# Optimization experiments

Measured on AMD Instinct MI355X. Metric: run time of the kernel, lower is better.

## Reference

```python
import jax, jax.numpy as jnp
import numpy as np

G = 8192          # graphs per hand side (PyG batch)
J_SRC = 17        # source-hand joints (transform: Linear(17*64, 13*64))
J_TGT = 13        # target-hand joints
NEG_SLOPE = 0.01  # F.leaky_relu default


def _chain_edge_index(J, num_graphs):
    # bidirectional chain tree per graph, block-diagonal batched like PyG
    p = np.arange(J - 1); c = np.arange(1, J)
    src = np.concatenate([p, c]); dst = np.concatenate([c, p])
    base = np.arange(num_graphs)[:, None] * J
    return jnp.asarray(np.stack([(src[None] + base).ravel(), (dst[None] + base).ravel()]), jnp.int32)


def _lin_init(key, o, i):
    k1, k2 = jax.random.split(key)
    s = 1.0 / np.sqrt(i)
    return (jax.random.uniform(k1, (o, i), jnp.float32, -s, s),
            jax.random.uniform(k2, (o,), jnp.float32, -s, s))


def setup_inputs() -> dict:
    key = jax.random.key(0)
    ks = iter(jax.random.split(key, 64))
    inp = {}
    Nl = G * J_SRC
    inp["l_hand_x"] = jax.random.normal(next(ks), (Nl, 3), jnp.float32)
    inp["r_hand_x"] = jax.random.normal(next(ks), (Nl, 3), jnp.float32)
    ei_src = _chain_edge_index(J_SRC, G)
    inp["l_hand_edge_index"] = ei_src
    inp["r_hand_edge_index"] = ei_src
    E_src = ei_src.shape[1]
    inp["l_hand_edge_attr"] = jax.random.normal(next(ks), (E_src, 3), jnp.float32)
    inp["r_hand_edge_attr"] = jax.random.normal(next(ks), (E_src, 3), jnp.float32)
    ei_t = _chain_edge_index(J_TGT, G)
    inp["hand_edge_index"] = ei_t
    inp["hand_edge_attr"] = jax.random.normal(next(ks), (ei_t.shape[1], 6), jnp.float32)
    Nt = G * J_TGT
    inp["hand_lower"] = -(jax.random.uniform(next(ks), (Nt, 1), jnp.float32) + 0.5)
    inp["hand_upper"] = jax.random.uniform(next(ks), (Nt, 1), jnp.float32) + 0.5
    inp["hand_offset"] = jax.random.normal(next(ks), (Nt, 3), jnp.float32) * 0.05
    ax = jax.random.normal(next(ks), (Nt, 3), jnp.float32)
    inp["hand_axis"] = ax / jnp.linalg.norm(ax, axis=-1, keepdims=True)
    par = np.concatenate([[-1], np.arange(J_TGT - 1)])  # chain: root then parents
    inp["hand_parent"] = jnp.asarray(np.tile(par, G), jnp.int32)
    inp["num_graphs"] = G
    dims = {"enc1_lin": (16, 9),  "enc1_up": (16, 3),
            "enc2_lin": (32, 35), "enc2_up": (32, 16),
            "enc3_lin": (64, 67), "enc3_up": (64, 32),
            "trans":    (13 * 64, 17 * 64),
            "dec1_lin": (32, 138), "dec1_up": (32, 66),
            "dec2_lin": (16, 70),  "dec2_up": (16, 32),
            "dec3_lin": (1, 38),   "dec3_up": (1, 16)}
    for n, (o, i) in dims.items():
        W, b = _lin_init(next(ks), o, i)
        inp[n + "_W"] = W; inp[n + "_b"] = b
    return inp


def _block(x, ei, ea, Wl, bl, Wu, bu):
    # SpatialBasicBlock: gather x_i/x_j, concat edge_attr, linear+leaky_relu,
    # scatter-add at target nodes, residual upsample of x.
    src, dst = ei[0], ei[1]
    z = jnp.concatenate([x[dst], x[src], ea], axis=-1)  # [E, 2*in+edge]
    m = jax.nn.leaky_relu(z @ Wl.T + bl, NEG_SLOPE)
    agg = jax.ops.segment_sum(m, dst, num_segments=x.shape[0])
    return agg + x @ Wu.T + bu


def _rodrigues(ax, ang):
    # rotation matrices about unit axis ax [...,3] by angle ang [...]
    c = jnp.cos(ang)[..., None, None]; s = jnp.sin(ang)[..., None, None]
    I = jnp.eye(3, dtype=ax.dtype)
    aa = ax[..., :, None] * ax[..., None, :]
    x, y, z = ax[..., 0], ax[..., 1], ax[..., 2]
    zero = jnp.zeros_like(x)
    K = jnp.stack([jnp.stack([zero, -z, y], -1),
                   jnp.stack([z, zero, -x], -1),
                   jnp.stack([-y, x, zero], -1)], -2)
    return c * I + (1 - c) * aa + s * K


def _fk(ang, parent, offset, axis, num_graphs, J):
    # forward kinematics along parent chain (parent[j] < j, root = -1)
    a = ang.reshape(num_graphs, J)
    off = offset.reshape(num_graphs, J, 3)
    ax = axis.reshape(num_graphs, J, 3)
    par = parent.reshape(num_graphs, J)[0]  # same topology in every graph
    Rl = _rodrigues(ax, a)                  # [G, J, 3, 3] local rotations
    I = jnp.eye(3, dtype=ang.dtype)
    pos = jnp.zeros((num_graphs, J, 3), ang.dtype)
    rot = jnp.zeros((num_graphs, J, 3, 3), ang.dtype)
    for j in range(J):  # J=13 fixed structural loop
        p = par[j]
        root = p < 0
        Rp = jnp.where(root, I, jnp.take(rot, p, axis=1))
        Pp = jnp.where(root, 0.0, jnp.take(pos, p, axis=1))
        pos = pos.at[:, j].set(Pp + jnp.einsum('gab,gb->ga', Rp, off[:, j]))
        rot = rot.at[:, j].set(jnp.einsum('gab,gbc->gac', Rp, Rl[:, j]))
    return pos.reshape(-1, 3)


def reference(l_hand_x, r_hand_x, l_hand_edge_index, r_hand_edge_index,
              l_hand_edge_attr, r_hand_edge_attr, hand_edge_index, hand_edge_attr,
              hand_lower, hand_upper, hand_offset, hand_axis, hand_parent, num_graphs,
              enc1_lin_W, enc1_lin_b, enc1_up_W, enc1_up_b,
              enc2_lin_W, enc2_lin_b, enc2_up_W, enc2_up_b,
              enc3_lin_W, enc3_lin_b, enc3_up_W, enc3_up_b,
              trans_W, trans_b,
              dec1_lin_W, dec1_lin_b, dec1_up_W, dec1_up_b,
              dec2_lin_W, dec2_lin_b, dec2_up_W, dec2_up_b,
              dec3_lin_W, dec3_lin_b, dec3_up_W, dec3_up_b):
    # ---- encode ----
    Nl = l_hand_x.shape[0]
    x = jnp.concatenate([l_hand_x, r_hand_x], axis=0)
    ei = jnp.concatenate([l_hand_edge_index, r_hand_edge_index + Nl], axis=1)
    ea = jnp.concatenate([l_hand_edge_attr, r_hand_edge_attr], axis=0)
    h = _block(x, ei, ea, enc1_lin_W, enc1_lin_b, enc1_up_W, enc1_up_b)
    h = _block(h, ei, ea, enc2_lin_W, enc2_lin_b, enc2_up_W, enc2_up_b)
    h = _block(h, ei, ea, enc3_lin_W, enc3_lin_b, enc3_up_W, enc3_up_b)
    G2 = 2 * num_graphs
    z = jnp.tanh(h.reshape(G2, -1) @ trans_W.T + trans_b).reshape(-1, 64)
    # ---- decode ----
    half = z.shape[0] // 2
    ei_t = jnp.concatenate([hand_edge_index, hand_edge_index + half], axis=1)
    ea_t = jnp.concatenate([hand_edge_attr, hand_edge_attr], axis=0)
    lower = jnp.concatenate([hand_lower, hand_lower], axis=0)
    upper = jnp.concatenate([hand_upper, hand_upper], axis=0)
    offset = jnp.concatenate([hand_offset, hand_offset], axis=0)
    axis = jnp.concatenate([hand_axis, hand_axis], axis=0)
    parent = jnp.concatenate([hand_parent, hand_parent], axis=0)
    xd = jnp.concatenate([z, lower, upper], axis=1)  # [2*G*13, 66]
    h = _block(xd, ei_t, ea_t, dec1_lin_W, dec1_lin_b, dec1_up_W, dec1_up_b)
    h = _block(h, ei_t, ea_t, dec2_lin_W, dec2_lin_b, dec2_up_W, dec2_up_b)
    ang = jnp.tanh(_block(h, ei_t, ea_t, dec3_lin_W, dec3_lin_b, dec3_up_W, dec3_up_b))
    ang = lower + (upper - lower) * (ang + 1) / 2
    pos = _fk(ang, parent, offset, axis, G2, J_TGT)
    hn = ang.shape[0] // 2
    return ang[:hn], pos[:hn], ang[hn:], pos[hn:]
```

## Files before the change

### kernel.cpp

```cpp
#include <hip/hip_runtime.h>
#include <math.h>


constexpr int G_NUM = 8192;
constexpr int JS = 17;
constexpr int JT = 13;
constexpr int N_ENC = 2 * G_NUM * JS;
constexpr int N_DEC = 2 * G_NUM * JT;
constexpr int G2 = 2 * G_NUM;
constexpr int HN = G_NUM * JT;
constexpr int K_TR = JS * 64;
constexpr int N_TR = JT * 64;

typedef unsigned short u16;
typedef u16   u16x8 __attribute__((ext_vector_type(8)));
typedef u16   u16x4 __attribute__((ext_vector_type(4)));
typedef float f32x4 __attribute__((ext_vector_type(4)));
typedef __bf16 bf16x8 __attribute__((ext_vector_type(8)));

__device__ __forceinline__ float lrelu(float v) { return v > 0.f ? v : 0.01f * v; }
__device__ __forceinline__ u16 f2bf(float f) {
    unsigned u = __float_as_uint(f);
    u += 0x7fff + ((u >> 16) & 1);
    return (u16)(u >> 16);
}
__device__ __forceinline__ float bf2f(u16 h) { return __uint_as_float((unsigned)h << 16); }

template<int K_MM, int C_IN_W, int C_OUT, int C_E, int J, int G, bool TAIL>
__global__ __launch_bounds__(256)
void block_mfma(const u16* __restrict__ xHi, const u16* __restrict__ xLo,
                const float* __restrict__ eaA, const float* __restrict__ eaB, int g_half,
                const float* __restrict__ lowv, const float* __restrict__ upv,
                const float* __restrict__ Wl, const float* __restrict__ bl,
                const float* __restrict__ Wu, const float* __restrict__ bu,
                u16* __restrict__ outHi, u16* __restrict__ outLo)
{
    constexpr int ROWS = G * J;
    constexpr int F = (ROWS + 15) / 16;
    constexpr int NCH = C_OUT / 16;
    constexpr int KF = K_MM / 32;
    constexpr int KPAD = K_MM + 8;
    constexpr int EAS = 2 * (J - 1) * C_E;
    constexpr int CTOT = 2 * C_IN_W + C_E;
    constexpr int CW = (C_IN_W < K_MM) ? C_IN_W : K_MM;
    constexpr int WGG = 4 * G;

    __shared__ __align__(16) u16 sWH[3 * C_OUT * KPAD], sWL[3 * C_OUT * KPAD];
    __shared__ float sEA[WGG * EAS];
    __shared__ float sWe[C_OUT * C_E];
    __shared__ float sBl[C_OUT], sBu[C_OUT];
    __shared__ float sTl[TAIL ? 6 * C_OUT : 1];
    __shared__ float sLow[TAIL ? WGG * J : 1], sUpp[TAIL ? WGG * J : 1];

    const int t = threadIdx.x;
    const int g0 = blockIdx.x * WGG;

    for (int i = t; i < 3 * C_OUT * K_MM; i += 256) {
        const int ch = i / K_MM, k = i % K_MM;
        const int p = ch / C_OUT, o = ch % C_OUT;
        float v = 0.f;
        if (k < CW) {
            if (p == 0)      v = Wl[o * CTOT + k];
            else if (p == 1) v = Wl[o * CTOT + C_IN_W + k];
            else             v = Wu[o * C_IN_W + k];
        }
        const u16 h = f2bf(v);
        sWH[ch * KPAD + k] = h;
        sWL[ch * KPAD + k] = f2bf(v - bf2f(h));
    }
    for (int i = t; i < WGG * EAS; i += 256) {
        const int lg = i / EAS, r = i % EAS;
        const int g = g0 + lg;
        sEA[i] = (g < g_half) ? eaA[(size_t)g * EAS + r]
                              : eaB[(size_t)(g - g_half) * EAS + r];
    }
    for (int i = t; i < C_OUT * C_E; i += 256)
        sWe[i] = Wl[(i / C_E) * CTOT + 2 * C_IN_W + (i % C_E)];
    if (t < C_OUT) { sBl[t] = bl[t]; sBu[t] = bu[t]; }
    if constexpr (TAIL) {
        if (t < C_OUT) {
            sTl[t * 6 + 0] = Wl[t * CTOT + K_MM];
            sTl[t * 6 + 1] = Wl[t * CTOT + K_MM + 1];
            sTl[t * 6 + 2] = Wl[t * CTOT + C_IN_W + K_MM];
            sTl[t * 6 + 3] = Wl[t * CTOT + C_IN_W + K_MM + 1];
            sTl[t * 6 + 4] = Wu[t * C_IN_W + K_MM];
            sTl[t * 6 + 5] = Wu[t * C_IN_W + K_MM + 1];
        }
        for (int i = t; i < WGG * J; i += 256) {
            const int lg = i / J, j = i % J;
            const int g = g0 + lg;
            const int ge = (g < g_half) ? g : g - g_half;
            sLow[i] = lowv[ge * J + j];
            sUpp[i] = upv[ge * J + j];
        }
    }
    __syncthreads();

    const int wv = t >> 6, lane = t & 63;
    const int col = lane & 15, kg = lane >> 4;
    const size_t baseNode = (size_t)(blockIdx.x * 4 + wv) * ROWS;
    const int lgB = wv * G;

    for (int ch = 0; ch < NCH; ++ch) {
        const int o = ch * 16 + col;
        bf16x8 wUh[KF], wUl[KF], wVh[KF], wVl[KF], wPh[KF], wPl[KF];
        #pragma unroll
        for (int kf = 0; kf < KF; ++kf) {
            wUh[kf] = *(const bf16x8*)&sWH[(0 * C_OUT + o) * KPAD + kf * 32 + kg * 8];
            wUl[kf] = *(const bf16x8*)&sWL[(0 * C_OUT + o) * KPAD + kf * 32 + kg * 8];
            wVh[kf] = *(const bf16x8*)&sWH[(1 * C_OUT + o) * KPAD + kf * 32 + kg * 8];
            wVl[kf] = *(const bf16x8*)&sWL[(1 * C_OUT + o) * KPAD + kf * 32 + kg * 8];
            wPh[kf] = *(const bf16x8*)&sWH[(2 * C_OUT + o) * KPAD + kf * 32 + kg * 8];
            wPl[kf] = *(const bf16x8*)&sWL[(2 * C_OUT + o) * KPAD + kf * 32 + kg * 8];
        }
        float we[C_E];
        #pragma unroll
        for (int k = 0; k < C_E; ++k) we[k] = sWe[o * C_E + k];
        const float blo = sBl[o], buo = sBu[o];
        float tl0 = 0, tl1 = 0, tl2 = 0, tl3 = 0, tl4 = 0, tl5 = 0;
        if constexpr (TAIL) {
            tl0 = sTl[o * 6 + 0]; tl1 = sTl[o * 6 + 1]; tl2 = sTl[o * 6 + 2];
            tl3 = sTl[o * 6 + 3]; tl4 = sTl[o * 6 + 4]; tl5 = sTl[o * 6 + 5];
        }

        f32x4 Vpp = {0,0,0,0}, Vp = {0,0,0,0};
        f32x4 Up = {0,0,0,0}, Pp = {0,0,0,0};
        #pragma unroll
        for (int f = 0; f <= F; ++f) {
            f32x4 Vc = {0,0,0,0}, Uc = {0,0,0,0}, Pc = {0,0,0,0};
            if (f < F) {
                const int nrow = f * 16 + col;
                const size_t nd = baseNode + (nrow < ROWS ? nrow : ROWS - 1);
                #pragma unroll
                for (int kf = 0; kf < KF; ++kf) {
                    const bf16x8 aH = *(const bf16x8*)&xHi[nd * K_MM + kf * 32 + kg * 8];
                    const bf16x8 aL = *(const bf16x8*)&xLo[nd * K_MM + kf * 32 + kg * 8];
                    Vc = __builtin_amdgcn_mfma_f32_16x16x32_bf16(aH, wVh[kf], Vc, 0, 0, 0);
                    Vc = __builtin_amdgcn_mfma_f32_16x16x32_bf16(aH, wVl[kf], Vc, 0, 0, 0);
                    Vc = __builtin_amdgcn_mfma_f32_16x16x32_bf16(aL, wVh[kf], Vc, 0, 0, 0);
                    Uc = __builtin_amdgcn_mfma_f32_16x16x32_bf16(aH, wUh[kf], Uc, 0, 0, 0);
                    Uc = __builtin_amdgcn_mfma_f32_16x16x32_bf16(aH, wUl[kf], Uc, 0, 0, 0);
                    Uc = __builtin_amdgcn_mfma_f32_16x16x32_bf16(aL, wUh[kf], Uc, 0, 0, 0);
                    Pc = __builtin_amdgcn_mfma_f32_16x16x32_bf16(aH, wPh[kf], Pc, 0, 0, 0);
                    Pc = __builtin_amdgcn_mfma_f32_16x16x32_bf16(aH, wPl[kf], Pc, 0, 0, 0);
                    Pc = __builtin_amdgcn_mfma_f32_16x16x32_bf16(aL, wPh[kf], Pc, 0, 0, 0);
                }
            }
            if (f >= 1) {
                const int fm = f - 1;
                const float vL0a = __shfl(Vpp[3], 48 + col);
                const float vL0b = __shfl(Vp[3], (lane - 16) & 63);
                const float vL0 = (kg == 0) ? vL0a : vL0b;
                const float vR3a = __shfl(Vc[0], col);
                const float vR3b = __shfl(Vp[0], (lane + 16) & 63);
                const float vR3 = (kg == 3) ? vR3a : vR3b;
                #pragma unroll
                for (int r = 0; r < 4; ++r) {
                    const int row = fm * 16 + kg * 4 + r;
                    const bool valid = row < ROWS;
                    const int jpos = row % J;
                    int gl = row / J; if (gl > G - 1) gl = G - 1;
                    const int lg = lgB + gl;
                    const bool h1m = valid && (jpos > 0);
                    const bool h2m = valid && (jpos < J - 1);
                    const int jm = jpos > 0 ? jpos - 1 : 0;
                    float e1 = 0.f, e2 = 0.f;
                    #pragma unroll
                    for (int k = 0; k < C_E; ++k) {
                        e1 = fmaf(we[k], sEA[lg * EAS + jm * C_E + k], e1);
                        e2 = fmaf(we[k], sEA[lg * EAS + (J - 1 + jpos) * C_E + k], e2);
                    }
                    float vL = (r == 0) ? vL0 : Vp[r - 1];
                    float vR = (r == 3) ? vR3 : Vp[r + 1];
                    float u = Up[r], p = Pp[r];
                    if constexpr (TAIL) {
                        const int jp = jpos < J - 1 ? jpos + 1 : J - 1;
                        u = fmaf(tl0, sLow[lg * J + jpos], u);
                        u = fmaf(tl1, sUpp[lg * J + jpos], u);
                        p = fmaf(tl4, sLow[lg * J + jpos], p);
                        p = fmaf(tl5, sUpp[lg * J + jpos], p);
                        vL = fmaf(tl2, sLow[lg * J + jm], vL);
                        vL = fmaf(tl3, sUpp[lg * J + jm], vL);
                        vR = fmaf(tl2, sLow[lg * J + jp], vR);
                        vR = fmaf(tl3, sUpp[lg * J + jp], vR);
                    }
                    const float m1 = u + vL + e1 + blo;
                    const float m2 = u + vR + e2 + blo;
                    const float res = p + buo + (h1m ? lrelu(m1) : 0.f) + (h2m ? lrelu(m2) : 0.f);
                    if (valid) {
                        const size_t node = baseNode + row;
                        const u16 hh = f2bf(res);
                        outHi[node * C_OUT + o] = hh;
                        outLo[node * C_OUT + o] = f2bf(res - bf2f(hh));
                    }
                }
            }
            Vpp = Vp; Vp = Vc; Up = Uc; Pp = Pc;
        }
    }
}

template<int C_IN, int C_OUT, int C_E, int J, int NN, int OPAD>
__global__ __launch_bounds__(256)
void block_small(const float* __restrict__ xA, const float* __restrict__ xB, int node_half,
                 const float* __restrict__ eaA, const float* __restrict__ eaB, int g_half,
                 const float* __restrict__ Wl, const float* __restrict__ bl,
                 const float* __restrict__ Wu, const float* __restrict__ bu,
                 u16* __restrict__ outHi, u16* __restrict__ outLo, int N)
{
    constexpr int CTOT = 2 * C_IN + C_E;
    constexpr int SOP = C_OUT + 1;
    constexpr int NPB = 256 / C_OUT;
    __shared__ float wl_T[CTOT * SOP];
    __shared__ float wu_T[C_IN * SOP];
    __shared__ float bl_s[C_OUT], bu_s[C_OUT];
    const int t = threadIdx.x;
    for (int i = t; i < C_OUT * CTOT; i += 256) { int oo = i / CTOT, kk = i % CTOT; wl_T[kk * SOP + oo] = Wl[i]; }
    for (int i = t; i < C_OUT * C_IN; i += 256) { int oo = i / C_IN, kk = i % C_IN; wu_T[kk * SOP + oo] = Wu[i]; }
    if (t < C_OUT) { bl_s[t] = bl[t]; bu_s[t] = bu[t]; }
    __syncthreads();

    const int o = t % C_OUT;
    const int s = t / C_OUT;
    const int nb = (blockIdx.x * NPB + s) * NN;
    float up[NN], m1[NN], m2[NN];
    #pragma unroll
    for (int i = 0; i < NN; ++i) { up[i] = bu_s[o]; m1[i] = bl_s[o]; m2[i] = bl_s[o]; }
    auto clampn = [&](int nd) { return nd < 0 ? 0 : (nd >= N ? N - 1 : nd); };

    for (int k = 0; k < C_IN; ++k) {
        const float w0 = wl_T[k * SOP + o];
        const float w1 = wl_T[(C_IN + k) * SOP + o];
        const float wuv = wu_T[k * SOP + o];
        float xs[NN + 2];
        #pragma unroll
        for (int i = 0; i < NN + 2; ++i) {
            const int nd = clampn(nb - 1 + i);
            xs[i] = (nd < node_half) ? xA[(size_t)nd * C_IN + k]
                                     : xB[(size_t)(nd - node_half) * C_IN + k];
        }
        #pragma unroll
        for (int nd = 0; nd < NN; ++nd) {
            up[nd] = fmaf(wuv, xs[nd + 1], up[nd]);
            m1[nd] = fmaf(w0, xs[nd + 1], m1[nd]);
            m1[nd] = fmaf(w1, xs[nd], m1[nd]);
            m2[nd] = fmaf(w0, xs[nd + 1], m2[nd]);
            m2[nd] = fmaf(w1, xs[nd + 2], m2[nd]);
        }
    }
    #pragma unroll
    for (int nd = 0; nd < NN; ++nd) {
        const int node = nb + nd;
        const int g = node / J;
        const int j = node - g * J;
        const bool has1 = (j > 0), has2 = (j < J - 1);
        const int geff = (g < g_half) ? g : g - g_half;
        const float* ea = (g < g_half) ? eaA : eaB;
        const ptrdiff_t e1 = ((ptrdiff_t)geff * 2 * (J - 1) + (j - 1)) * C_E;
        const ptrdiff_t e2 = ((ptrdiff_t)geff * 2 * (J - 1) + (J - 1) + j) * C_E;
        float a1 = m1[nd], a2 = m2[nd];
        #pragma unroll
        for (int k = 0; k < C_E; ++k) {
            const float w = wl_T[(2 * C_IN + k) * SOP + o];
            if (has1) a1 = fmaf(w, ea[e1 + k], a1);
            if (has2) a2 = fmaf(w, ea[e2 + k], a2);
        }
        const float v = up[nd] + (has1 ? lrelu(a1) : 0.f) + (has2 ? lrelu(a2) : 0.f);
        const u16 hh = f2bf(v);
        outHi[(size_t)node * OPAD + o] = hh;
        outLo[(size_t)node * OPAD + o] = f2bf(v - bf2f(hh));
        if (OPAD > C_OUT) {
            outHi[(size_t)node * OPAD + o + C_OUT] = 0;
            outLo[(size_t)node * OPAD + o + C_OUT] = 0;
        }
    }
}

__global__ __launch_bounds__(256)
void trans_mfma(const u16* __restrict__ aHi, const u16* __restrict__ aLo,
                const float* __restrict__ W, const float* __restrict__ bias,
                u16* __restrict__ zHi, u16* __restrict__ zLo)
{
    constexpr int BK = 32, AS = 40, BS = 40;
    __shared__ __align__(16) u16 sAH[128 * AS], sAL[128 * AS];
    __shared__ __align__(16) u16 sBH[64 * BS],  sBL[64 * BS];
    const int t = threadIdx.x;
    const int bm = blockIdx.x * 128, bn = blockIdx.y * 64;
    const int lane = t & 63, w = t >> 6;
    const int wm = w >> 1, wn = w & 1;
    const int lr = lane & 15, kg = lane >> 4;
    const int ar = t >> 2, ac = (t & 3) * 8;
    const int br = t >> 3, bc = (t & 7) * 4;

    u16x8 rA[4];
    float4 rW[2];
    auto gload = [&](int k0) {
        const size_t oa = (size_t)(bm + ar) * K_TR + k0 + ac;
        rA[0] = *(const u16x8*)&aHi[oa];
        rA[1] = *(const u16x8*)&aLo[oa];
        rA[2] = *(const u16x8*)&aHi[oa + (size_t)64 * K_TR];
        rA[3] = *(const u16x8*)&aLo[oa + (size_t)64 * K_TR];
        rW[0] = *(const float4*)&W[(size_t)(bn + br) * K_TR + k0 + bc];
        rW[1] = *(const float4*)&W[(size_t)(bn + 32 + br) * K_TR + k0 + bc];
    };

    f32x4 acc[4][2];
    #pragma unroll
    for (int m = 0; m < 4; ++m)
        #pragma unroll
        for (int n = 0; n < 2; ++n) acc[m][n] = f32x4{0.f, 0.f, 0.f, 0.f};

    gload(0);
    for (int k0 = 0; k0 < K_TR; k0 += BK) {
        __syncthreads();
        *(u16x8*)&sAH[ar * AS + ac] = rA[0];
        *(u16x8*)&sAL[ar * AS + ac] = rA[1];
        *(u16x8*)&sAH[(64 + ar) * AS + ac] = rA[2];
        *(u16x8*)&sAL[(64 + ar) * AS + ac] = rA[3];
        #pragma unroll
        for (int p = 0; p < 2; ++p) {
            const int row = p * 32 + br;
            const float fv[4] = {rW[p].x, rW[p].y, rW[p].z, rW[p].w};
            u16x4 hq, lq;
            #pragma unroll
            for (int i = 0; i < 4; ++i) {
                const u16 h = f2bf(fv[i]);
                hq[i] = h;
                lq[i] = f2bf(fv[i] - bf2f(h));
            }
            *(u16x4*)&sBH[row * BS + bc] = hq;
            *(u16x4*)&sBL[row * BS + bc] = lq;
        }
        __syncthreads();
        if (k0 + BK < K_TR) gload(k0 + BK);
        bf16x8 ah[4], al[4], bh[2], bl2[2];
        #pragma unroll
        for (int m = 0; m < 4; ++m) {
            const int r = wm * 64 + m * 16 + lr;
            ah[m] = *(const bf16x8*)&sAH[r * AS + kg * 8];
            al[m] = *(const bf16x8*)&sAL[r * AS + kg * 8];
        }
        #pragma unroll
        for (int n = 0; n < 2; ++n) {
            const int r = wn * 32 + n * 16 + lr;
            bh[n]  = *(const bf16x8*)&sBH[r * BS + kg * 8];
            bl2[n] = *(const bf16x8*)&sBL[r * BS + kg * 8];
        }
        #pragma unroll
        for (int m = 0; m < 4; ++m)
            #pragma unroll
            for (int n = 0; n < 2; ++n) {
                acc[m][n] = __builtin_amdgcn_mfma_f32_16x16x32_bf16(ah[m], bh[n],  acc[m][n], 0, 0, 0);
                acc[m][n] = __builtin_amdgcn_mfma_f32_16x16x32_bf16(ah[m], bl2[n], acc[m][n], 0, 0, 0);
                acc[m][n] = __builtin_amdgcn_mfma_f32_16x16x32_bf16(al[m], bh[n],  acc[m][n], 0, 0, 0);
            }
    }
    #pragma unroll
    for (int n = 0; n < 2; ++n) {
        const int colz = bn + wn * 32 + n * 16 + lr;
        const float bv = bias[colz];
        #pragma unroll
        for (int m = 0; m < 4; ++m)
            #pragma unroll
            for (int r = 0; r < 4; ++r) {
                const int row = bm + wm * 64 + m * 16 + kg * 4 + r;
                const float v = tanhf(acc[m][n][r] + bv);
                const size_t idx = (size_t)row * N_TR + colz;
                const u16 hh = f2bf(v);
                zHi[idx] = hh;
                zLo[idx] = f2bf(v - bf2f(hh));
            }
    }
}

__global__ __launch_bounds__(256)
void dec3_kernel(const u16* __restrict__ xHi, const u16* __restrict__ xLo,
                 const float* __restrict__ ea,
                 const float* __restrict__ Wl, const float* __restrict__ bl,
                 const float* __restrict__ Wu, const float* __restrict__ bu,
                 const float* __restrict__ lowv, const float* __restrict__ upv,
                 float* __restrict__ dout, int N)
{
    const int node = blockIdx.x * 256 + threadIdx.x;
    if (node >= N) return;
    const int g = node / JT;
    const int j = node - g * JT;
    const int geff = (g >= G_NUM) ? g - G_NUM : g;
    const bool has1 = (j > 0), has2 = (j < JT - 1);
    float m1 = bl[0], m2 = m1, up = bu[0];
    auto xv = [&](int nd, int k) -> float {
        return bf2f(xHi[(size_t)nd * 16 + k]) + bf2f(xLo[(size_t)nd * 16 + k]);
    };
    #pragma unroll
    for (int k = 0; k < 16; ++k) {
        const float xd = xv(node, k);
        up = fmaf(Wu[k], xd, up);
        const float w0 = Wl[k];
        m1 = fmaf(w0, xd, m1);
        m2 = fmaf(w0, xd, m2);
        const float w1 = Wl[16 + k];
        if (has1) m1 = fmaf(w1, xv(node - 1, k), m1);
        if (has2) m2 = fmaf(w1, xv(node + 1, k), m2);
    }
    const int e1 = (geff * 24 + (j - 1)) * 6;
    const int e2 = (geff * 24 + 12 + j) * 6;
    #pragma unroll
    for (int k = 0; k < 6; ++k) {
        const float w = Wl[32 + k];
        if (has1) m1 = fmaf(w, ea[e1 + k], m1);
        if (has2) m2 = fmaf(w, ea[e2 + k], m2);
    }
    const float v = up + (has1 ? lrelu(m1) : 0.f) + (has2 ? lrelu(m2) : 0.f);
    const int idx = (node >= HN) ? node - HN : node;
    const float lo = lowv[idx], hi = upv[idx];
    const float a = lo + (hi - lo) * (tanhf(v) + 1.f) * 0.5f;
    if (node < HN) dout[node] = a;
    else           dout[4 * HN + node - HN] = a;
}

__global__ __launch_bounds__(256)
void fk_kernel(float* __restrict__ dout,
               const float* __restrict__ offset, const float* __restrict__ axis)
{
    const int g2 = blockIdx.x * 256 + threadIdx.x;
    if (g2 >= G2) return;
    float R[9];
    float px = 0.f, py = 0.f, pz = 0.f;
    for (int j = 0; j < JT; ++j) {
        const int node = g2 * JT + j;
        const int idx = (node >= HN) ? node - HN : node;
        const float a = (node < HN) ? dout[node] : dout[4 * HN + node - HN];
        const float ax = axis[idx * 3], ay = axis[idx * 3 + 1], az = axis[idx * 3 + 2];
        const float ox = offset[idx * 3], oy = offset[idx * 3 + 1], oz = offset[idx * 3 + 2];
        const float c = cosf(a), s = sinf(a), ic = 1.f - c;
        const float L[9] = {
            c + ic * ax * ax,      ic * ax * ay - s * az, ic * ax * az + s * ay,
            ic * ay * ax + s * az, c + ic * ay * ay,      ic * ay * az - s * ax,
            ic * az * ax - s * ay, ic * az * ay + s * ax, c + ic * az * az };
        if (j == 0) {
            px = ox; py = oy; pz = oz;
            #pragma unroll
            for (int q = 0; q < 9; ++q) R[q] = L[q];
        } else {
            px += R[0] * ox + R[1] * oy + R[2] * oz;
            py += R[3] * ox + R[4] * oy + R[5] * oz;
            pz += R[6] * ox + R[7] * oy + R[8] * oz;
            float T[9];
            #pragma unroll
            for (int r = 0; r < 3; ++r)
                #pragma unroll
                for (int cc = 0; cc < 3; ++cc)
                    T[r * 3 + cc] = R[r * 3] * L[cc] + R[r * 3 + 1] * L[3 + cc] + R[r * 3 + 2] * L[6 + cc];
            #pragma unroll
            for (int q = 0; q < 9; ++q) R[q] = T[q];
        }
        const int pbase = (node < HN) ? (HN + node * 3) : (5 * HN + (node - HN) * 3);
        dout[pbase] = px; dout[pbase + 1] = py; dout[pbase + 2] = pz;
    }
}

extern "C" void kernel_launch(void* const* d_in, const int* in_sizes, int n_in,
                              void* d_out, int out_size, void* d_ws, size_t ws_size,
                              hipStream_t stream)
{
    const float* l_x  = (const float*)d_in[0];
    const float* r_x  = (const float*)d_in[1];
    const float* l_ea = (const float*)d_in[4];
    const float* r_ea = (const float*)d_in[5];
    const float* ea_t = (const float*)d_in[7];
    const float* lowv = (const float*)d_in[8];
    const float* upv  = (const float*)d_in[9];
    const float* offs = (const float*)d_in[10];
    const float* axis = (const float*)d_in[11];
    const float* e1lW = (const float*)d_in[14]; const float* e1lB = (const float*)d_in[15];
    const float* e1uW = (const float*)d_in[16]; const float* e1uB = (const float*)d_in[17];
    const float* e2lW = (const float*)d_in[18]; const float* e2lB = (const float*)d_in[19];
    const float* e2uW = (const float*)d_in[20]; const float* e2uB = (const float*)d_in[21];
    const float* e3lW = (const float*)d_in[22]; const float* e3lB = (const float*)d_in[23];
    const float* e3uW = (const float*)d_in[24]; const float* e3uB = (const float*)d_in[25];
    const float* trW  = (const float*)d_in[26]; const float* trB  = (const float*)d_in[27];
    const float* d1lW = (const float*)d_in[28]; const float* d1lB = (const float*)d_in[29];
    const float* d1uW = (const float*)d_in[30]; const float* d1uB = (const float*)d_in[31];
    const float* d2lW = (const float*)d_in[32]; const float* d2lB = (const float*)d_in[33];
    const float* d2uW = (const float*)d_in[34]; const float* d2uB = (const float*)d_in[35];
    const float* d3lW = (const float*)d_in[36]; const float* d3lB = (const float*)d_in[37];
    const float* d3uW = (const float*)d_in[38]; const float* d3uB = (const float*)d_in[39];

    char* ws = (char*)d_ws;
    u16* h1H  = (u16*)(ws + 0);          u16* h1L  = (u16*)(ws + 17825792);
    u16* h2H  = (u16*)(ws + 71303168);   u16* h2L  = (u16*)(ws + 89128960);
    u16* aH   = (u16*)(ws + 0);          u16* aL   = (u16*)(ws + 35651584);
    u16* zzH  = (u16*)(ws + 71303168);   u16* zzL  = (u16*)(ws + 98566144);
    u16* hd1H = (u16*)(ws + 0);          u16* hd1L = (u16*)(ws + 13631488);
    u16* hd2H = (u16*)(ws + 27262976);   u16* hd2L = (u16*)(ws + 34078720);
    float* outp = (float*)d_out;

    block_small<3, 16, 3, JS, 4, 32><<<N_ENC / 64, 256, 0, stream>>>(
        l_x, r_x, G_NUM * JS, l_ea, r_ea, G_NUM,
        e1lW, e1lB, e1uW, e1uB, h1H, h1L, N_ENC);
    block_mfma<32, 16, 32, 3, JS, 4, false><<<1024, 256, 0, stream>>>(
        h1H, h1L, l_ea, r_ea, G_NUM, nullptr, nullptr,
        e2lW, e2lB, e2uW, e2uB, h2H, h2L);
    block_mfma<32, 32, 64, 3, JS, 4, false><<<1024, 256, 0, stream>>>(
        h2H, h2L, l_ea, r_ea, G_NUM, nullptr, nullptr,
        e3lW, e3lB, e3uW, e3uB, aH, aL);
    trans_mfma<<<dim3(G2 / 128, N_TR / 64), 256, 0, stream>>>(aH, aL, trW, trB, zzH, zzL);
    block_mfma<64, 66, 32, 6, JT, 4, true><<<1024, 256, 0, stream>>>(
        zzH, zzL, ea_t, ea_t, G_NUM, lowv, upv,
        d1lW, d1lB, d1uW, d1uB, hd1H, hd1L);
    block_mfma<32, 32, 16, 6, JT, 4, false><<<1024, 256, 0, stream>>>(
        hd1H, hd1L, ea_t, ea_t, G_NUM, nullptr, nullptr,
        d2lW, d2lB, d2uW, d2uB, hd2H, hd2L);
    dec3_kernel<<<(N_DEC + 255) / 256, 256, 0, stream>>>(
        hd2H, hd2L, ea_t, d3lW, d3lB, d3uW, d3uB, lowv, upv, outp, N_DEC);
    fk_kernel<<<(G2 + 255) / 256, 256, 0, stream>>>(outp, offs, axis);
}
```

Before: 516.7 us.

## Double-buffer trans GEMM weights, load A directly to registers, fuse dec3 with FK

The transform GEMM now stages only the converted weight tile in double-buffered shared memory and loads the A operand fragments straight from global memory into registers in MFMA layout. This removes the A shared-memory round trip and one barrier per K step. Separately, the last decoder layer is fused into the forward-kinematics kernel: one thread per graph walks its 13 joints with a sliding window of neighbour rows, which removes a launch and the write-then-reread of the angles. The cost is that the fused kernel has only 16384 threads, so it has low parallelism and its per-thread row loads are strided and uncoalesced.

```diff
diff --git a/kernel.cpp b/kernel.cpp
--- a/kernel.cpp
+++ b/kernel.cpp
@@ -276,33 +276,68 @@
     }
 }
 
+__device__ __forceinline__ void trans_step(const u16* __restrict__ sWHb,
+                                           const u16* __restrict__ sWLb,
+                                           const u16x8* __restrict__ a,
+                                           int wn, int lr, int kg, f32x4 acc[4][2])
+{
+    bf16x8 bh[2], bl2[2];
+    #pragma unroll
+    for (int n = 0; n < 2; ++n) {
+        const int r = wn * 32 + n * 16 + lr;
+        bh[n]  = *(const bf16x8*)&sWHb[r * 40 + kg * 8];
+        bl2[n] = *(const bf16x8*)&sWLb[r * 40 + kg * 8];
+    }
+    #pragma unroll
+    for (int m = 0; m < 4; ++m) {
+        const bf16x8 ah = __builtin_bit_cast(bf16x8, a[2 * m]);
+        const bf16x8 al = __builtin_bit_cast(bf16x8, a[2 * m + 1]);
+        #pragma unroll
+        for (int n = 0; n < 2; ++n) {
+            acc[m][n] = __builtin_amdgcn_mfma_f32_16x16x32_bf16(ah, bh[n],  acc[m][n], 0, 0, 0);
+            acc[m][n] = __builtin_amdgcn_mfma_f32_16x16x32_bf16(ah, bl2[n], acc[m][n], 0, 0, 0);
+            acc[m][n] = __builtin_amdgcn_mfma_f32_16x16x32_bf16(al, bh[n],  acc[m][n], 0, 0, 0);
+        }
+    }
+}
+
 __global__ __launch_bounds__(256)
 void trans_mfma(const u16* __restrict__ aHi, const u16* __restrict__ aLo,
                 const float* __restrict__ W, const float* __restrict__ bias,
                 u16* __restrict__ zHi, u16* __restrict__ zLo)
 {
-    constexpr int BK = 32, AS = 40, BS = 40;
-    __shared__ __align__(16) u16 sAH[128 * AS], sAL[128 * AS];
-    __shared__ __align__(16) u16 sBH[64 * BS],  sBL[64 * BS];
-    const int t = threadIdx.x;
+    constexpr int NI = K_TR / 32;
+    __shared__ __align__(16) u16 sWH[2][64 * 40], sWL[2][64 * 40];
+    const int t = threadIdx.x, lane = t & 63, w = t >> 6;
+    const int wm = w >> 1, wn = w & 1, lr = lane & 15, kg = lane >> 4;
     const int bm = blockIdx.x * 128, bn = blockIdx.y * 64;
-    const int lane = t & 63, w = t >> 6;
-    const int wm = w >> 1, wn = w & 1;
-    const int lr = lane & 15, kg = lane >> 4;
-    const int ar = t >> 2, ac = (t & 3) * 8;
-    const int br = t >> 3, bc = (t & 7) * 4;
-
-    u16x8 rA[4];
-    float4 rW[2];
-    auto gload = [&](int k0) {
-        const size_t oa = (size_t)(bm + ar) * K_TR + k0 + ac;
-        rA[0] = *(const u16x8*)&aHi[oa];
-        rA[1] = *(const u16x8*)&aLo[oa];
-        rA[2] = *(const u16x8*)&aHi[oa + (size_t)64 * K_TR];
-        rA[3] = *(const u16x8*)&aLo[oa + (size_t)64 * K_TR];
-        rW[0] = *(const float4*)&W[(size_t)(bn + br) * K_TR + k0 + bc];
-        rW[1] = *(const float4*)&W[(size_t)(bn + 32 + br) * K_TR + k0 + bc];
+    const int swr = t >> 2, swc = (t & 3) * 8;
+
+    auto stageW = [&](int i, int buf) {
+        const int k0 = i * 32;
+        const float4 f0 = *(const float4*)&W[(size_t)(bn + swr) * K_TR + k0 + swc];
+        const float4 f1 = *(const float4*)&W[(size_t)(bn + swr) * K_TR + k0 + swc + 4];
+        const float fv[8] = {f0.x, f0.y, f0.z, f0.w, f1.x, f1.y, f1.z, f1.w};
+        u16x8 hq, lq;
+        #pragma unroll
+        for (int j = 0; j < 8; ++j) {
+            const u16 h = f2bf(fv[j]);
+            hq[j] = h;
+            lq[j] = f2bf(fv[j] - bf2f(h));
+        }
+        *(u16x8*)&sWH[buf][swr * 40 + swc] = hq;
+        *(u16x8*)&sWL[buf][swr * 40 + swc] = lq;
     };
+    u16x8 aA[8], aB[8];
+    auto gloadA = [&](int i, u16x8* dst) {
+        const int k0 = i * 32;
+        #pragma unroll
+        for (int m = 0; m < 4; ++m) {
+            const size_t off = (size_t)(bm + wm * 64 + m * 16 + lr) * K_TR + k0 + kg * 8;
+            dst[2 * m]     = *(const u16x8*)&aHi[off];
+            dst[2 * m + 1] = *(const u16x8*)&aLo[off];
+        }
+    };
 
     f32x4 acc[4][2];
     #pragma unroll
@@ -310,51 +345,18 @@
         #pragma unroll
         for (int n = 0; n < 2; ++n) acc[m][n] = f32x4{0.f, 0.f, 0.f, 0.f};
 
-    gload(0);
-    for (int k0 = 0; k0 < K_TR; k0 += BK) {
+    stageW(0, 0);
+    gloadA(0, aA);
+    __syncthreads();
+    for (int i = 0; i < NI; i += 2) {
+        if (i + 1 < NI) { stageW(i + 1, 1); gloadA(i + 1, aB); }
+        trans_step(sWH[0], sWL[0], aA, wn, lr, kg, acc);
         __syncthreads();
-        *(u16x8*)&sAH[ar * AS + ac] = rA[0];
-        *(u16x8*)&sAL[ar * AS + ac] = rA[1];
-        *(u16x8*)&sAH[(64 + ar) * AS + ac] = rA[2];
-        *(u16x8*)&sAL[(64 + ar) * AS + ac] = rA[3];
-        #pragma unroll
-        for (int p = 0; p < 2; ++p) {
-            const int row = p * 32 + br;
-            const float fv[4] = {rW[p].x, rW[p].y, rW[p].z, rW[p].w};
-            u16x4 hq, lq;
-            #pragma unroll
-            for (int i = 0; i < 4; ++i) {
-                const u16 h = f2bf(fv[i]);
-                hq[i] = h;
-                lq[i] = f2bf(fv[i] - bf2f(h));
-            }
-            *(u16x4*)&sBH[row * BS + bc] = hq;
-            *(u16x4*)&sBL[row * BS + bc] = lq;
-        }
+        if (i + 2 < NI) { stageW(i + 2, 0); gloadA(i + 2, aA); }
+        trans_step(sWH[1], sWL[1], aB, wn, lr, kg, acc);
         __syncthreads();
-        if (k0 + BK < K_TR) gload(k0 + BK);
-        bf16x8 ah[4], al[4], bh[2], bl2[2];
-        #pragma unroll
-        for (int m = 0; m < 4; ++m) {
-            const int r = wm * 64 + m * 16 + lr;
-            ah[m] = *(const bf16x8*)&sAH[r * AS + kg * 8];
-            al[m] = *(const bf16x8*)&sAL[r * AS + kg * 8];
-        }
-        #pragma unroll
-        for (int n = 0; n < 2; ++n) {
-            const int r = wn * 32 + n * 16 + lr;
-            bh[n]  = *(const bf16x8*)&sBH[r * BS + kg * 8];
-            bl2[n] = *(const bf16x8*)&sBL[r * BS + kg * 8];
-        }
-        #pragma unroll
-        for (int m = 0; m < 4; ++m)
-            #pragma unroll
-            for (int n = 0; n < 2; ++n) {
-                acc[m][n] = __builtin_amdgcn_mfma_f32_16x16x32_bf16(ah[m], bh[n],  acc[m][n], 0, 0, 0);
-                acc[m][n] = __builtin_amdgcn_mfma_f32_16x16x32_bf16(ah[m], bl2[n], acc[m][n], 0, 0, 0);
-                acc[m][n] = __builtin_amdgcn_mfma_f32_16x16x32_bf16(al[m], bh[n],  acc[m][n], 0, 0, 0);
-            }
-    }
+    }
+
     #pragma unroll
     for (int n = 0; n < 2; ++n) {
         const int colz = bn + wn * 32 + n * 16 + lr;
@@ -374,62 +376,69 @@
 }
 
 __global__ __launch_bounds__(256)
-void dec3_kernel(const u16* __restrict__ xHi, const u16* __restrict__ xLo,
-                 const float* __restrict__ ea,
-                 const float* __restrict__ Wl, const float* __restrict__ bl,
-                 const float* __restrict__ Wu, const float* __restrict__ bu,
-                 const float* __restrict__ lowv, const float* __restrict__ upv,
-                 float* __restrict__ dout, int N)
-{
-    const int node = blockIdx.x * 256 + threadIdx.x;
-    if (node >= N) return;
-    const int g = node / JT;
-    const int j = node - g * JT;
-    const int geff = (g >= G_NUM) ? g - G_NUM : g;
-    const bool has1 = (j > 0), has2 = (j < JT - 1);
-    float m1 = bl[0], m2 = m1, up = bu[0];
-    auto xv = [&](int nd, int k) -> float {
-        return bf2f(xHi[(size_t)nd * 16 + k]) + bf2f(xLo[(size_t)nd * 16 + k]);
-    };
-    #pragma unroll
-    for (int k = 0; k < 16; ++k) {
-        const float xd = xv(node, k);
-        up = fmaf(Wu[k], xd, up);
-        const float w0 = Wl[k];
-        m1 = fmaf(w0, xd, m1);
-        m2 = fmaf(w0, xd, m2);
-        const float w1 = Wl[16 + k];
-        if (has1) m1 = fmaf(w1, xv(node - 1, k), m1);
-        if (has2) m2 = fmaf(w1, xv(node + 1, k), m2);
-    }
-    const int e1 = (geff * 24 + (j - 1)) * 6;
-    const int e2 = (geff * 24 + 12 + j) * 6;
-    #pragma unroll
-    for (int k = 0; k < 6; ++k) {
-        const float w = Wl[32 + k];
-        if (has1) m1 = fmaf(w, ea[e1 + k], m1);
-        if (has2) m2 = fmaf(w, ea[e2 + k], m2);
-    }
-    const float v = up + (has1 ? lrelu(m1) : 0.f) + (has2 ? lrelu(m2) : 0.f);
-    const int idx = (node >= HN) ? node - HN : node;
-    const float lo = lowv[idx], hi = upv[idx];
-    const float a = lo + (hi - lo) * (tanhf(v) + 1.f) * 0.5f;
-    if (node < HN) dout[node] = a;
-    else           dout[4 * HN + node - HN] = a;
-}
-
-__global__ __launch_bounds__(256)
-void fk_kernel(float* __restrict__ dout,
-               const float* __restrict__ offset, const float* __restrict__ axis)
+void dec3fk_kernel(const u16* __restrict__ xHi, const u16* __restrict__ xLo,
+                   const float* __restrict__ ea,
+                   const float* __restrict__ Wl, const float* __restrict__ bl,
+                   const float* __restrict__ Wu, const float* __restrict__ bu,
+                   const float* __restrict__ lowv, const float* __restrict__ upv,
+                   const float* __restrict__ offset, const float* __restrict__ axis,
+                   float* __restrict__ dout)
 {
     const int g2 = blockIdx.x * 256 + threadIdx.x;
     if (g2 >= G2) return;
+    const int geff = (g2 >= G_NUM) ? g2 - G_NUM : g2;
+    const bool rightH = (g2 >= G_NUM);
+
+    auto loadrow = [&](int nd, float* x) {
+        const u16x8 h0 = *(const u16x8*)&xHi[(size_t)nd * 16];
+        const u16x8 h1 = *(const u16x8*)&xHi[(size_t)nd * 16 + 8];
+        const u16x8 l0 = *(const u16x8*)&xLo[(size_t)nd * 16];
+        const u16x8 l1 = *(const u16x8*)&xLo[(size_t)nd * 16 + 8];
+        #pragma unroll
+        for (int k = 0; k < 8; ++k) {
+            x[k]     = bf2f(h0[k]) + bf2f(l0[k]);
+            x[k + 8] = bf2f(h1[k]) + bf2f(l1[k]);
+        }
+    };
+
+    float xprev[16], xcur[16], xnext[16];
+    #pragma unroll
+    for (int k = 0; k < 16; ++k) xprev[k] = 0.f;
+    loadrow(g2 * JT, xcur);
+    loadrow(g2 * JT + 1, xnext);
+
     float R[9];
     float px = 0.f, py = 0.f, pz = 0.f;
     for (int j = 0; j < JT; ++j) {
         const int node = g2 * JT + j;
-        const int idx = (node >= HN) ? node - HN : node;
-        const float a = (node < HN) ? dout[node] : dout[4 * HN + node - HN];
+        const bool has1 = (j > 0), has2 = (j < JT - 1);
+        float m1 = bl[0], m2 = m1, up = bu[0];
+        #pragma unroll
+        for (int k = 0; k < 16; ++k) {
+            const float xd = xcur[k];
+            up = fmaf(Wu[k], xd, up);
+            const float w0 = Wl[k];
+            m1 = fmaf(w0, xd, m1);
+            m2 = fmaf(w0, xd, m2);
+            const float w1 = Wl[16 + k];
+            m1 = fmaf(w1, xprev[k], m1);
+            m2 = fmaf(w1, xnext[k], m2);
+        }
+        const int e1 = (geff * 24 + (j - 1)) * 6;
+        const int e2 = (geff * 24 + 12 + j) * 6;
+        #pragma unroll
+        for (int k = 0; k < 6; ++k) {
+            const float ww = Wl[32 + k];
+            if (has1) m1 = fmaf(ww, ea[e1 + k], m1);
+            if (has2) m2 = fmaf(ww, ea[e2 + k], m2);
+        }
+        const float v = up + (has1 ? lrelu(m1) : 0.f) + (has2 ? lrelu(m2) : 0.f);
+        const int idx = geff * JT + j;
+        const float lo = lowv[idx], hi = upv[idx];
+        const float a = lo + (hi - lo) * (tanhf(v) + 1.f) * 0.5f;
+        if (!rightH) dout[node] = a;
+        else         dout[4 * HN + idx] = a;
+
         const float ax = axis[idx * 3], ay = axis[idx * 3 + 1], az = axis[idx * 3 + 2];
         const float ox = offset[idx * 3], oy = offset[idx * 3 + 1], oz = offset[idx * 3 + 2];
         const float c = cosf(a), s = sinf(a), ic = 1.f - c;
@@ -454,8 +463,13 @@
             #pragma unroll
             for (int q = 0; q < 9; ++q) R[q] = T[q];
         }
-        const int pbase = (node < HN) ? (HN + node * 3) : (5 * HN + (node - HN) * 3);
+        const int pbase = (!rightH) ? (HN + node * 3) : (5 * HN + idx * 3);
         dout[pbase] = px; dout[pbase + 1] = py; dout[pbase + 2] = pz;
+
+        #pragma unroll
+        for (int k = 0; k < 16; ++k) { xprev[k] = xcur[k]; xcur[k] = xnext[k]; }
+        const int nn = node + 2 < N_DEC ? node + 2 : N_DEC - 1;
+        if (j < JT - 1) loadrow(nn, xnext);
     }
 }
 
@@ -511,7 +525,6 @@
     block_mfma<32, 32, 16, 6, JT, 4, false><<<1024, 256, 0, stream>>>(
         hd1H, hd1L, ea_t, ea_t, G_NUM, nullptr, nullptr,
         d2lW, d2lB, d2uW, d2uB, hd2H, hd2L);
-    dec3_kernel<<<(N_DEC + 255) / 256, 256, 0, stream>>>(
-        hd2H, hd2L, ea_t, d3lW, d3lB, d3uW, d3uB, lowv, upv, outp, N_DEC);
-    fk_kernel<<<(G2 + 255) / 256, 256, 0, stream>>>(outp, offs, axis);
-}
+    dec3fk_kernel<<<(G2 + 255) / 256, 256, 0, stream>>>(
+        hd2H, hd2L, ea_t, d3lW, d3lB, d3uW, d3uB, lowv, upv, offs, axis, outp);
+}
```

Result: slower. 633.8 us (+22.7%).
